# Optimization experiments

Measured on AMD Instinct MI355X. Metric: run time of the kernel, lower is better.

## Reference

```python
import jax, jax.numpy as jnp
import numpy as np

N_HEADS = 16
D_HEAD = 64
IGNORE = -100000.0


def setup_inputs() -> dict:
    key = jax.random.key(0)
    ks = jax.random.split(key, 5)
    B, S, D = 2, 2048, 1024
    return {
        "residual": jax.random.normal(ks[0], (B, S, D), dtype=jnp.float32),
        "q": jax.random.normal(ks[1], (B, S, D), dtype=jnp.float32),
        "k": jax.random.normal(ks[2], (B, S, D), dtype=jnp.float32),
        "v": jax.random.normal(ks[3], (B, S, D), dtype=jnp.float32),
        "W_O": jax.random.normal(ks[4], (N_HEADS, D_HEAD, D), dtype=jnp.float32) * 0.02,
        "b_O": jnp.zeros((D,), dtype=jnp.float32),
    }


def reference(residual, q, k, v, W_O, b_O):
    B, S, _ = q.shape
    attn_scale = np.sqrt(D_HEAD).astype(np.float32)  # use_attn_scale=True
    # split heads: [..., pos, (h d)] -> [..., pos, h, d]
    qh = q.reshape(B, S, N_HEADS, D_HEAD)
    kh = k.reshape(B, S, N_HEADS, D_HEAD)
    vh = v.reshape(B, S, N_HEADS, D_HEAD)
    # scores: [..., head, query_pos, key_pos]
    scores = jnp.einsum("bqhd,bkhd->bhqk", qh, kh) / attn_scale
    causal = jnp.tril(jnp.ones((S, S), dtype=bool))
    scores = jnp.where(causal, scores, jnp.float32(IGNORE))
    pattern = jax.nn.softmax(scores, axis=-1)
    # weighted sum of values: [..., query_pos, head, d_head]
    z = jnp.einsum("bkhd,bhqk->bqhd", vh, pattern)
    out = jnp.einsum("bqhd,hdm->bqm", z, W_O) + b_O
    return (residual, out)
```

## Files before the change

kernel.cpp:

```cpp
#include <hip/hip_runtime.h>

#define B_ 2
#define S_ 2048
#define D_ 1024
#define H_ 16
#define DH_ 64
#define NP_ 2048

typedef short v8s __attribute__((ext_vector_type(8)));
typedef float v4f __attribute__((ext_vector_type(4)));
typedef float v16f __attribute__((ext_vector_type(16)));
typedef unsigned int v2u __attribute__((ext_vector_type(2)));
typedef unsigned int v4u __attribute__((ext_vector_type(4)));
typedef unsigned int uint32;

__device__ inline short f2bf(float f) {
  unsigned u = __float_as_uint(f);
  u = (u + 0x7FFFu + ((u >> 16) & 1u)) >> 16;
  return (short)u;
}

__device__ inline unsigned pk_bf16(float lo, float hi) {
  unsigned r;
  asm("v_cvt_pk_bf16_f32 %0, %1, %2" : "=v"(r) : "v"(lo), "v"(hi));
  return r;
}

__device__ inline void gll16(const void* g, void* l) {
  __builtin_amdgcn_global_load_lds(
      (const __attribute__((address_space(1))) void*)g,
      (__attribute__((address_space(3))) void*)l, 16, 0, 0);
}

__global__ __launch_bounds__(256) void cvt_all_kernel(
    const float* __restrict__ k, short* __restrict__ kb,
    const float* __restrict__ v, short* __restrict__ vt,
    const float* __restrict__ w, short* __restrict__ wt) {
  __shared__ short t[64][64 + 8];
  int bid = blockIdx.x;
  int tid = threadIdx.x;
  if (bid < 2048) {
    int i = bid * 256 + tid;
    float4 a = ((const float4*)k)[2 * i];
    float4 b = ((const float4*)k)[2 * i + 1];
    v8s o;
    o[0] = f2bf(a.x); o[1] = f2bf(a.y); o[2] = f2bf(a.z); o[3] = f2bf(a.w);
    o[4] = f2bf(b.x); o[5] = f2bf(b.y); o[6] = f2bf(b.z); o[7] = f2bf(b.w);
    ((v8s*)kb)[i] = o;
    return;
  }
  int r = tid >> 2, c16 = (tid & 3) * 16;
  if (bid < 3072) {
    int id = bid - 2048;
    int st = id & 31;
    int bh = id >> 5;
    int b = bh >> 4, h = bh & 15;
    const float* vp = v + ((size_t)(b * S_ + st * 64 + r)) * D_ + h * DH_ + c16;
    for (int i = 0; i < 16; i += 4) {
      float4 a = *(const float4*)(vp + i);
      t[r][c16 + i + 0] = f2bf(a.x);
      t[r][c16 + i + 1] = f2bf(a.y);
      t[r][c16 + i + 2] = f2bf(a.z);
      t[r][c16 + i + 3] = f2bf(a.w);
    }
    __syncthreads();
    short* op = vt + ((size_t)((b * H_ + h) * DH_ + r)) * S_ + st * 64 + c16;
    v8s o0, o1;
    for (int j = 0; j < 8; ++j) { o0[j] = t[c16 + j][r]; o1[j] = t[c16 + 8 + j][r]; }
    *(v8s*)op = o0;
    *(v8s*)(op + 8) = o1;
  } else {
    int id = bid - 3072;
    int tk = id & 15, tm = id >> 4;
    const float* wp = w + (size_t)(tk * 64 + r) * D_ + tm * 64 + c16;
    for (int i = 0; i < 16; i += 4) {
      float4 a = *(const float4*)(wp + i);
      t[r][c16 + i + 0] = f2bf(a.x);
      t[r][c16 + i + 1] = f2bf(a.y);
      t[r][c16 + i + 2] = f2bf(a.z);
      t[r][c16 + i + 3] = f2bf(a.w);
    }
    __syncthreads();
    short* op = wt + (size_t)(tm * 64 + r) * D_ + tk * 64 + c16;
    v8s o0, o1;
    for (int j = 0; j < 8; ++j) { o0[j] = t[c16 + j][r]; o1[j] = t[c16 + 8 + j][r]; }
    *(v8s*)op = o0;
    *(v8s*)(op + 8) = o1;
  }
}

template <int SPLITS>
__global__ __launch_bounds__(256, 4) void attn_kernel(
    const float* __restrict__ q, const short* __restrict__ kbf,
    const short* __restrict__ vtb, uint32* __restrict__ Opart,
    float* __restrict__ Lsum, const float* __restrict__ residual,
    float* __restrict__ res_out) {
  int bid = blockIdx.x;
  int bh = bid & 31;
  int sp = (SPLITS == 2) ? ((bid >> 5) & 1) : 0;
  int t = (SPLITS == 2) ? (bid >> 6) : (bid >> 5);
  int g = t >> 2;
  int qt = (g == 0) ? 15 - t : (g == 1) ? t - 4 : (g == 2) ? 19 - t : t - 8;
  int b = bh >> 4, h = bh & 15;

  const int nt = 2 * qt + 2;
  const int t0 = (SPLITS == 2 && sp == 1) ? qt + 1 : 0;
  const int t1 = (SPLITS == 2 && sp == 0) ? qt : nt - 1;

  int tid = threadIdx.x;
  int wave = tid >> 6, lane = tid & 63;
  int l31 = lane & 31, h32 = lane >> 5;

  __shared__ short Klds[2][64][64];
  __shared__ short Vlds[2][64][64];

  const int qrow0 = qt * 128 + wave * 32;
  const int lr8 = lane >> 3;
  const int scol = ((lane & 7) ^ lr8) << 3;

  const int sw = wave & 1;
  const short* kbase = kbf + (size_t)b * S_ * D_ + h * DH_ +
                       (size_t)(sw * 8 + lr8) * D_ + scol;
  const short* vbase = vtb + (size_t)(b * H_ + h) * DH_ * S_ +
                       (size_t)(sw * 8 + lr8) * S_ + scol;

  v8s qf[4];
  {
    const float* qp = q + (size_t)(b * S_ + qrow0 + l31) * D_ + h * DH_ + h32 * 8;
    const float sc = 0.125f * 1.44269504f;
#pragma unroll
    for (int d4 = 0; d4 < 4; ++d4) {
      float4 x = *(const float4*)(qp + d4 * 16);
      float4 y = *(const float4*)(qp + d4 * 16 + 4);
      v8s tq;
      tq[0] = f2bf(x.x * sc); tq[1] = f2bf(x.y * sc);
      tq[2] = f2bf(x.z * sc); tq[3] = f2bf(x.w * sc);
      tq[4] = f2bf(y.x * sc); tq[5] = f2bf(y.y * sc);
      tq[6] = f2bf(y.z * sc); tq[7] = f2bf(y.w * sc);
      qf[d4] = tq;
    }
  }

  v16f O0, O1;
#pragma unroll
  for (int r = 0; r < 16; ++r) { O0[r] = 0.f; O1[r] = 0.f; }
  float L = 0.f;
  const int swz = (l31 & 7) << 3;

  auto stage = [&](int tt, int buf) {
    if (wave < 2) {
      const short* kp = kbase + (size_t)(tt * 64) * D_;
#pragma unroll
      for (int i = 0; i < 4; ++i)
        gll16(kp + (size_t)(i * 16) * D_, &Klds[buf][i * 16 + sw * 8][0]);
    } else {
      const short* vp = vbase + tt * 64;
#pragma unroll
      for (int i = 0; i < 4; ++i)
        gll16(vp + (size_t)(i * 16) * S_, &Vlds[buf][i * 16 + sw * 8][0]);
    }
  };

  stage(t0, t0 & 1);

  for (int s = t0; s <= t1; ++s) {
    int cur = s & 1;
    if (s < t1) {
      stage(s + 1, cur ^ 1);
      asm volatile("s_waitcnt vmcnt(4)" ::: "memory");
    } else {
      asm volatile("s_waitcnt vmcnt(0)" ::: "memory");
    }
    __builtin_amdgcn_sched_barrier(0);
    __builtin_amdgcn_s_barrier();
    __builtin_amdgcn_sched_barrier(0);

    int kb = s * 64;
    bool fullskip = (kb >= qrow0 + 32);
    if (!fullskip) {
      bool skip1 = (kb >= qrow0);
      bool msk = (kb + 63 > qrow0);

      __builtin_amdgcn_s_setprio(1);
      v16f S0, S1;
#pragma unroll
      for (int r = 0; r < 16; ++r) { S0[r] = 0.f; S1[r] = 0.f; }
#pragma unroll
      for (int d4 = 0; d4 < 4; ++d4) {
        v8s kf = *(const v8s*)&Klds[cur][l31][(((d4 << 1) | h32) << 3) ^ swz];
        S0 = __builtin_amdgcn_mfma_f32_32x32x16_bf16(kf, qf[d4], S0, 0, 0, 0);
      }
      if (!skip1) {
#pragma unroll
        for (int d4 = 0; d4 < 4; ++d4) {
          v8s kf = *(const v8s*)&Klds[cur][32 + l31][(((d4 << 1) | h32) << 3) ^ swz];
          S1 = __builtin_amdgcn_mfma_f32_32x32x16_bf16(kf, qf[d4], S1, 0, 0, 0);
        }
      }
      __builtin_amdgcn_s_setprio(0);

      int qg = qrow0 + l31;
      if (msk) {
#pragma unroll
        for (int r = 0; r < 16; ++r) {
          int kl = kb + (r & 3) + 8 * (r >> 2) + 4 * h32;
          if (kl > qg) S0[r] = -1e30f;
        }
        if (!skip1) {
#pragma unroll
          for (int r = 0; r < 16; ++r) {
            int kl = kb + 32 + (r & 3) + 8 * (r >> 2) + 4 * h32;
            if (kl > qg) S1[r] = -1e30f;
          }
        }
      }

      float rs = 0.f;
      unsigned pw0[8], pw1[8];
#pragma unroll
      for (int r = 0; r < 16; ++r) {
        S0[r] = __builtin_amdgcn_exp2f(S0[r]);
        rs += S0[r];
      }
#pragma unroll
      for (int w = 0; w < 8; ++w) pw0[w] = pk_bf16(S0[2 * w], S0[2 * w + 1]);
      if (!skip1) {
#pragma unroll
        for (int r = 0; r < 16; ++r) {
          S1[r] = __builtin_amdgcn_exp2f(S1[r]);
          rs += S1[r];
        }
#pragma unroll
        for (int w = 0; w < 8; ++w) pw1[w] = pk_bf16(S1[2 * w], S1[2 * w + 1]);
      }
      rs += __shfl_xor(rs, 32);
      L += rs;

      __builtin_amdgcn_s_setprio(1);
#pragma unroll
      for (int ks = 0; ks < 2; ++ks) {
        v2u a = __builtin_amdgcn_permlane32_swap(pw0[ks * 4 + 0], pw0[ks * 4 + 2], false, false);
        v2u c = __builtin_amdgcn_permlane32_swap(pw0[ks * 4 + 1], pw0[ks * 4 + 3], false, false);
        v4u fw; fw.x = a.x; fw.y = c.x; fw.z = a.y; fw.w = c.y;
        v8s pb = __builtin_bit_cast(v8s, fw);
        v8s vf0 = *(const v8s*)&Vlds[cur][l31][(((ks << 1) | h32) << 3) ^ swz];
        O0 = __builtin_amdgcn_mfma_f32_32x32x16_bf16(vf0, pb, O0, 0, 0, 0);
        v8s vf1 = *(const v8s*)&Vlds[cur][32 + l31][(((ks << 1) | h32) << 3) ^ swz];
        O1 = __builtin_amdgcn_mfma_f32_32x32x16_bf16(vf1, pb, O1, 0, 0, 0);
      }
      if (!skip1) {
#pragma unroll
        for (int ks = 0; ks < 2; ++ks) {
          v2u a = __builtin_amdgcn_permlane32_swap(pw1[ks * 4 + 0], pw1[ks * 4 + 2], false, false);
          v2u c = __builtin_amdgcn_permlane32_swap(pw1[ks * 4 + 1], pw1[ks * 4 + 3], false, false);
          v4u fw; fw.x = a.x; fw.y = c.x; fw.z = a.y; fw.w = c.y;
          v8s pb = __builtin_bit_cast(v8s, fw);
          v8s vf0 = *(const v8s*)&Vlds[cur][l31][((((ks + 2) << 1) | h32) << 3) ^ swz];
          O0 = __builtin_amdgcn_mfma_f32_32x32x16_bf16(vf0, pb, O0, 0, 0, 0);
          v8s vf1 = *(const v8s*)&Vlds[cur][32 + l31][((((ks + 2) << 1) | h32) << 3) ^ swz];
          O1 = __builtin_amdgcn_mfma_f32_32x32x16_bf16(vf1, pb, O1, 0, 0, 0);
        }
      }
      __builtin_amdgcn_s_setprio(0);
    }

    __builtin_amdgcn_sched_barrier(0);
    __builtin_amdgcn_s_barrier();
    __builtin_amdgcn_sched_barrier(0);
  }

  int p = bh * 64 + qt * 4 + wave;
  uint32* Op = Opart + ((size_t)(sp * NP_ + p)) * 1024;
#pragma unroll
  for (int w = 0; w < 8; ++w) {
    int dpair = 4 * (w >> 1) + (w & 1) + 2 * h32;
    Op[dpair * 32 + l31] = pk_bf16(O0[2 * w], O0[2 * w + 1]);
    Op[(16 + dpair) * 32 + l31] = pk_bf16(O1[2 * w], O1[2 * w + 1]);
  }
  if (h32 == 0) Lsum[(size_t)(sp * NP_ + p) * 32 + l31] = L;

  {
    constexpr int F4 = (SPLITS == 2) ? 4 : 8;
    const float4* rs_ = (const float4*)residual;
    float4* rd_ = (float4*)res_out;
    size_t base = (size_t)bid * (256 * F4) + tid;
#pragma unroll
    for (int j = 0; j < F4; ++j) rd_[base + j * 256] = rs_[base + j * 256];
  }
}

template <int SPLITS>
__global__ __launch_bounds__(128) void merge_kernel(
    const uint32* __restrict__ Opart, const float* __restrict__ Lsum,
    short* __restrict__ z) {
  int p = blockIdx.x;
  int tid = threadIdx.x;
  int qq = tid & 31, g = tid >> 5;

  float Lt = Lsum[(size_t)p * 32 + qq];
  if constexpr (SPLITS == 2) Lt += Lsum[((size_t)NP_ + p) * 32 + qq];
  float f = 1.f / Lt;

  __shared__ uint32 T[32][33];
#pragma unroll
  for (int j = 0; j < 8; ++j) {
    int dp = g * 8 + j;
    uint32 u0 = Opart[(size_t)p * 1024 + dp * 32 + qq];
    float lo = __uint_as_float(u0 << 16);
    float hi = __uint_as_float(u0 & 0xFFFF0000u);
    if constexpr (SPLITS == 2) {
      uint32 u1 = Opart[((size_t)NP_ + p) * 1024 + dp * 32 + qq];
      lo += __uint_as_float(u1 << 16);
      hi += __uint_as_float(u1 & 0xFFFF0000u);
    }
    T[qq][dp] = pk_bf16(lo * f, hi * f);
  }
  __syncthreads();
  int q2 = tid >> 2, c = (tid & 3) * 8;
  int srow = (p & 63) * 32 + q2;
  int b = p >> 10, h = (p >> 6) & 15;
  uint32* zp = (uint32*)z + ((size_t)(b * S_ + srow)) * (D_ / 2) + h * 32 + c;
#pragma unroll
  for (int j = 0; j < 8; ++j) zp[j] = T[q2][c + j];
}

__global__ __launch_bounds__(256) void proj_kernel(
    const short* __restrict__ z, const short* __restrict__ wt,
    const float* __restrict__ bias, float* __restrict__ out) {
  int bid = blockIdx.x;
  int bm = bid & 31, bn = bid >> 5;
  int tid = threadIdx.x;
  int wave = tid >> 6, lane = tid & 63, lh = lane >> 4, ll = lane & 15;
  int wr = wave >> 1, wc = wave & 1;

  __shared__ short Al[2][128][64];
  __shared__ short Bl[2][128][64];

  const int r8 = lane >> 3;
  const int scol = ((lane & 7) ^ r8) << 3;

  v4f acc[4][4];
#pragma unroll
  for (int m = 0; m < 4; ++m)
#pragma unroll
    for (int n = 0; n < 4; ++n) acc[m][n] = (v4f){0.f, 0.f, 0.f, 0.f};

  auto stage = [&](int kb, int bbuf) {
#pragma unroll
    for (int i = 0; i < 4; ++i) {
      int c = wave * 4 + i;
      gll16(z + (size_t)(bm * 128 + c * 8 + r8) * D_ + kb + scol, &Al[bbuf][c * 8][0]);
    }
#pragma unroll
    for (int i = 0; i < 4; ++i) {
      int c = wave * 4 + i;
      gll16(wt + (size_t)(bn * 128 + c * 8 + r8) * D_ + kb + scol, &Bl[bbuf][c * 8][0]);
    }
  };

  stage(0, 0);
  __syncthreads();

  for (int kt = 0; kt < D_ / 64; ++kt) {
    int bbuf = kt & 1;
    if (kt + 1 < D_ / 64) stage((kt + 1) * 64, bbuf ^ 1);
    v8s af[4][2], bf[4][2];
#pragma unroll
    for (int m = 0; m < 4; ++m) {
      int row = wr * 64 + m * 16 + ll;
#pragma unroll
      for (int c = 0; c < 2; ++c)
        af[m][c] = *(const v8s*)&Al[bbuf][row][(((c << 2) | lh) ^ (ll & 7)) << 3];
    }
#pragma unroll
    for (int n = 0; n < 4; ++n) {
      int row = wc * 64 + n * 16 + ll;
#pragma unroll
      for (int c = 0; c < 2; ++c)
        bf[n][c] = *(const v8s*)&Bl[bbuf][row][(((c << 2) | lh) ^ (ll & 7)) << 3];
    }
#pragma unroll
    for (int m = 0; m < 4; ++m)
#pragma unroll
      for (int n = 0; n < 4; ++n)
#pragma unroll
        for (int c = 0; c < 2; ++c)
          acc[m][n] = __builtin_amdgcn_mfma_f32_16x16x32_bf16(af[m][c], bf[n][c], acc[m][n], 0, 0, 0);
    __syncthreads();
  }

#pragma unroll
  for (int m = 0; m < 4; ++m) {
    int gr = bm * 128 + wr * 64 + m * 16 + lh * 4;
#pragma unroll
    for (int n = 0; n < 4; ++n) {
      int gc = bn * 128 + wc * 64 + n * 16 + ll;
      float bo = bias[gc];
#pragma unroll
      for (int r = 0; r < 4; ++r)
        out[(size_t)(gr + r) * D_ + gc] = acc[m][n][r] + bo;
    }
  }
}

extern "C" void kernel_launch(void* const* d_in, const int* in_sizes, int n_in,
                              void* d_out, int out_size, void* d_ws, size_t ws_size,
                              hipStream_t stream) {
  const float* residual = (const float*)d_in[0];
  const float* q = (const float*)d_in[1];
  const float* k = (const float*)d_in[2];
  const float* v = (const float*)d_in[3];
  const float* W = (const float*)d_in[4];
  const float* bO = (const float*)d_in[5];
  float* out = (float*)d_out;

  const size_t half = (size_t)B_ * S_ * D_;
  char* ws = (char*)d_ws;
  short* kbf = (short*)ws;
  short* vtb = kbf + half;
  short* wtb = vtb + half;
  char* pbase = (char*)(wtb + (size_t)D_ * D_);
  const size_t opart_b = (size_t)NP_ * 1024 * 4;
  const size_t l_b = (size_t)NP_ * 32 * 4;
  const size_t base_b = (size_t)pbase - (size_t)ws;
  short* z = kbf;

  cvt_all_kernel<<<3328, 256, 0, stream>>>(k, kbf, v, vtb, W, wtb);

  if (ws_size >= base_b + 2 * (opart_b + l_b)) {
    uint32* Opart = (uint32*)pbase;
    float* Lsum = (float*)(pbase + 2 * opart_b);
    attn_kernel<2><<<1024, 256, 0, stream>>>(q, kbf, vtb, Opart, Lsum, residual, out);
    merge_kernel<2><<<NP_, 128, 0, stream>>>(Opart, Lsum, z);
  } else {
    uint32* Opart = (uint32*)pbase;
    float* Lsum = (float*)(pbase + opart_b);
    attn_kernel<1><<<512, 256, 0, stream>>>(q, kbf, vtb, Opart, Lsum, residual, out);
    merge_kernel<1><<<NP_, 128, 0, stream>>>(Opart, Lsum, z);
  }
  proj_kernel<<<256, 256, 0, stream>>>(z, wtb, bO, out + half);
}
```

Before: 68.31 us.

## Fuse split-KV merge into attention kernel via per-tile atomic counters

Each attention block atomically increments a per-tile counter after writing its partial output and row sums. The last-arriving split reads both partials, normalizes them and writes bf16 z directly, so the separate merge kernel is no longer launched. A memset of the counters is added, z moves to its own workspace region, and the merge stores become strided per-lane writes rather than transposed through shared memory.

```diff
diff --git a/kernel.cpp b/kernel.cpp
--- a/kernel.cpp
+++ b/kernel.cpp
@@ -93,7 +93,8 @@
 __global__ __launch_bounds__(256, 4) void attn_kernel(
     const float* __restrict__ q, const short* __restrict__ kbf,
     const short* __restrict__ vtb, uint32* __restrict__ Opart,
-    float* __restrict__ Lsum, const float* __restrict__ residual,
+    float* __restrict__ Lsum, uint32* __restrict__ cnt,
+    short* __restrict__ z, const float* __restrict__ residual,
     float* __restrict__ res_out) {
   int bid = blockIdx.x;
   int bh = bid & 31;
@@ -279,6 +280,35 @@
   }
   if (h32 == 0) Lsum[(size_t)(sp * NP_ + p) * 32 + l31] = L;
 
+  __threadfence();
+  unsigned old = 0;
+  if (lane == 0) old = atomicAdd(&cnt[p], 1u);
+  old = __shfl(old, 0);
+  if (old == SPLITS - 1) {
+    __threadfence();
+    int qq = lane & 31, halfd = lane >> 5;
+    float Lt = Lsum[(size_t)p * 32 + qq];
+    if constexpr (SPLITS == 2) Lt += Lsum[((size_t)NP_ + p) * 32 + qq];
+    float f = 1.f / Lt;
+    int srow = (p & 63) * 32 + qq;
+    int bb = p >> 10, hh = (p >> 6) & 15;
+    uint32* zp = (uint32*)z + ((size_t)(bb * S_ + srow)) * (D_ / 2) + hh * 32 + halfd * 16;
+    const uint32* s0 = Opart + (size_t)p * 1024 + qq;
+#pragma unroll
+    for (int j = 0; j < 16; ++j) {
+      int dp = halfd * 16 + j;
+      uint32 u0 = s0[dp * 32];
+      float lo = __uint_as_float(u0 << 16);
+      float hi = __uint_as_float(u0 & 0xFFFF0000u);
+      if constexpr (SPLITS == 2) {
+        uint32 u1 = s0[(size_t)NP_ * 1024 + dp * 32];
+        lo += __uint_as_float(u1 << 16);
+        hi += __uint_as_float(u1 & 0xFFFF0000u);
+      }
+      zp[j] = pk_bf16(lo * f, hi * f);
+    }
+  }
+
   {
     constexpr int F4 = (SPLITS == 2) ? 4 : 8;
     const float4* rs_ = (const float4*)residual;
@@ -289,7 +319,6 @@
   }
 }
 
-template <int SPLITS>
 __global__ __launch_bounds__(128) void merge_kernel(
     const uint32* __restrict__ Opart, const float* __restrict__ Lsum,
     short* __restrict__ z) {
@@ -298,7 +327,6 @@
   int qq = tid & 31, g = tid >> 5;
 
   float Lt = Lsum[(size_t)p * 32 + qq];
-  if constexpr (SPLITS == 2) Lt += Lsum[((size_t)NP_ + p) * 32 + qq];
   float f = 1.f / Lt;
 
   __shared__ uint32 T[32][33];
@@ -308,11 +336,6 @@
     uint32 u0 = Opart[(size_t)p * 1024 + dp * 32 + qq];
     float lo = __uint_as_float(u0 << 16);
     float hi = __uint_as_float(u0 & 0xFFFF0000u);
-    if constexpr (SPLITS == 2) {
-      uint32 u1 = Opart[((size_t)NP_ + p) * 1024 + dp * 32 + qq];
-      lo += __uint_as_float(u1 << 16);
-      hi += __uint_as_float(u1 & 0xFFFF0000u);
-    }
     T[qq][dp] = pk_bf16(lo * f, hi * f);
   }
   __syncthreads();
@@ -423,20 +446,28 @@
   const size_t opart_b = (size_t)NP_ * 1024 * 4;
   const size_t l_b = (size_t)NP_ * 32 * 4;
   const size_t base_b = (size_t)pbase - (size_t)ws;
-  short* z = kbf;
 
   cvt_all_kernel<<<3328, 256, 0, stream>>>(k, kbf, v, vtb, W, wtb);
 
-  if (ws_size >= base_b + 2 * (opart_b + l_b)) {
+  if (ws_size >= base_b + 2 * (opart_b + l_b) + half * 2 + NP_ * 4) {
     uint32* Opart = (uint32*)pbase;
     float* Lsum = (float*)(pbase + 2 * opart_b);
-    attn_kernel<2><<<1024, 256, 0, stream>>>(q, kbf, vtb, Opart, Lsum, residual, out);
-    merge_kernel<2><<<NP_, 128, 0, stream>>>(Opart, Lsum, z);
+    short* z = (short*)(pbase + 2 * (opart_b + l_b));
+    uint32* cnt = (uint32*)(z + half);
+    hipMemsetAsync(cnt, 0, NP_ * 4, stream);
+    attn_kernel<2><<<1024, 256, 0, stream>>>(q, kbf, vtb, Opart, Lsum, cnt, z,
+                                             residual, out);
+    proj_kernel<<<256, 256, 0, stream>>>(z, wtb, bO, out + half);
   } else {
     uint32* Opart = (uint32*)pbase;
     float* Lsum = (float*)(pbase + opart_b);
-    attn_kernel<1><<<512, 256, 0, stream>>>(q, kbf, vtb, Opart, Lsum, residual, out);
-    merge_kernel<1><<<NP_, 128, 0, stream>>>(Opart, Lsum, z);
-  }
-  proj_kernel<<<256, 256, 0, stream>>>(z, wtb, bO, out + half);
-}
+    uint32* cnt = (uint32*)(pbase + opart_b + l_b);
+    short* z = kbf;
+    hipMemsetAsync(cnt, 0, NP_ * 4, stream);
+    attn_kernel<1><<<512, 256, 0, stream>>>(q, kbf, vtb, Opart, Lsum, cnt,
+                                            (short*)(pbase + opart_b + l_b + NP_ * 4),
+                                            residual, out);
+    merge_kernel<<<NP_, 128, 0, stream>>>(Opart, Lsum, z);
+    proj_kernel<<<256, 256, 0, stream>>>(z, wtb, bO, out + half);
+  }
+}
```

After: 265.0 us. 3.88x slower.
